# Kernel optimization log

Hardware: AMD Instinct MI355X
Metric: run time of the kernel (lower is better)

Reference implementation:

```python
import jax, jax.numpy as jnp
import numpy as np

N = 20000
E = 320000
IN = 256
H = 4
C = 64
NEG_SLOPE = 0.2


def setup_inputs() -> dict:
    key = jax.random.key(0)
    ks = jax.random.split(key, 12)
    HC = H * C

    def w(k, shape, fan_in):
        return jax.random.normal(k, shape, dtype=jnp.float32) / np.sqrt(fan_in)

    x = jax.random.normal(ks[0], (N, IN), dtype=jnp.float32)
    edge_index = jax.random.randint(ks[1], (2, E), 0, N, dtype=jnp.int64)
    return {
        "x": x,
        "edge_index": edge_index,
        "Wl1": w(ks[2], (IN, HC), IN),
        "Wr1": w(ks[3], (IN, HC), IN),
        "att1": w(ks[4], (H, C), C),
        "b1": jnp.zeros((HC,), dtype=jnp.float32),
        "Wl2": w(ks[5], (HC, HC), HC),
        "Wr2": w(ks[6], (HC, HC), HC),
        "att2": w(ks[7], (H, C), C),
        "b2": jnp.zeros((HC,), dtype=jnp.float32),
        "Wfc": w(ks[8], (HC, 2), HC),
        "bfc": jnp.zeros((2,), dtype=jnp.float32),
    }


def _gatv2(x, src, dst, Wl, Wr, att, b):
    """GATv2Conv (concat=True, share_weights=False), inference (no dropout)."""
    n = x.shape[0]
    xl = (x @ Wl).reshape(n, H, C)  # source-side projection
    xr = (x @ Wr).reshape(n, H, C)  # target-side projection
    # per-edge GATv2 score: a^T LeakyReLU(xl_j + xr_i)
    e = jax.nn.leaky_relu(xl[src] + xr[dst], NEG_SLOPE)      # [E, H, C]
    score = jnp.einsum("ehc,hc->eh", e, att)                 # [E, H]
    # segment softmax over incoming edges of each target node
    smax = jax.ops.segment_max(score, dst, num_segments=n)   # [N, H]
    ex = jnp.exp(score - smax[dst])
    denom = jax.ops.segment_sum(ex, dst, num_segments=n)     # [N, H]
    alpha = ex / denom[dst]                                  # [E, H]
    # scatter-aggregate messages (source projections weighted by alpha)
    out = jax.ops.segment_sum(alpha[:, :, None] * xl[src], dst, num_segments=n)
    return out.reshape(n, H * C) + b


def reference(x, edge_index, Wl1, Wr1, att1, b1, Wl2, Wr2, att2, b2, Wfc, bfc):
    n = x.shape[0]
    # add_self_loops=True (PyG default)
    loop = jnp.arange(n, dtype=edge_index.dtype)
    src = jnp.concatenate([edge_index[0], loop])
    dst = jnp.concatenate([edge_index[1], loop])

    h = _gatv2(x, src, dst, Wl1, Wr1, att1, b1)
    h = jax.nn.relu(h)
    h = _gatv2(h, src, dst, Wl2, Wr2, att2, b2)
    h = jax.nn.relu(h)
    g = jnp.mean(h, axis=0, keepdims=True)  # [1, H*C]
    return g @ Wfc + bfc                    # [1, 2]
```

## Files before the change

kernel.cpp:

```cpp
#include <hip/hip_runtime.h>
#include <hip/hip_bf16.h>
#include <math.h>

#define Nn 20000
#define Ee 320000
#define INF_ 256
#define Hh 4
#define Cc 64
#define HC 256
#define NB_ 79
#define NEG_SLOPE 0.2f

using frag16 = __attribute__((ext_vector_type(8))) short;
using f32x4  = __attribute__((ext_vector_type(4))) float;

__device__ __forceinline__ void async16(const void* g, void* l) {
    __builtin_amdgcn_global_load_lds(
        (const __attribute__((address_space(1))) unsigned int*)g,
        (__attribute__((address_space(3))) unsigned int*)l,
        16, 0, 0);
}


__global__ void init_deg(int* deg, float* gpart, int n) {
    int i = blockIdx.x * blockDim.x + threadIdx.x;
    if (i < n) deg[i] = 1;
    if (i < 32 * 256) gpart[i] = 0.f;
}

__global__ void hist_kernel(const int* __restrict__ dst, int ne, int* deg) {
    int e = blockIdx.x * blockDim.x + threadIdx.x;
    if (e < ne) atomicAdd(&deg[dst[e]], 1);
}

__global__ __launch_bounds__(256) void scan1(const int* __restrict__ deg,
                                             int* __restrict__ excl,
                                             int* __restrict__ bsum, int n) {
    int tid = threadIdx.x;
    int gid = blockIdx.x * 256 + tid;
    int lane = tid & 63;
    int v = (gid < n) ? deg[gid] : 0;
    int x = v;
    #pragma unroll
    for (int off = 1; off < 64; off <<= 1) {
        int y = __shfl_up(x, off, 64);
        if (lane >= off) x += y;
    }
    __shared__ int wsum[4];
    if (lane == 63) wsum[tid >> 6] = x;
    __syncthreads();
    int wadd = 0;
    for (int w = 0; w < (tid >> 6); ++w) wadd += wsum[w];
    int incl = x + wadd;
    if (gid < n) excl[gid] = incl - v;
    if (tid == 255) bsum[blockIdx.x] = incl;
}

__global__ void scan2(const int* __restrict__ bsum, int* __restrict__ boff, int nb) {
    int lane = threadIdx.x;
    int carry = 0;
    for (int base = 0; base < nb; base += 64) {
        int i = base + lane;
        int v = (i < nb) ? bsum[i] : 0;
        int x = v;
        #pragma unroll
        for (int off = 1; off < 64; off <<= 1) {
            int y = __shfl_up(x, off, 64);
            if (lane >= off) x += y;
        }
        if (i < nb) boff[i] = carry + x - v;
        carry += __shfl(x, 63, 64);
    }
    if (lane == 0) boff[nb] = carry;
}

__global__ void scan_add(int* __restrict__ row_start, int* __restrict__ cursor,
                         const int* __restrict__ boff, int n, int nb) {
    int gid = blockIdx.x * blockDim.x + threadIdx.x;
    if (gid < n) {
        int v = row_start[gid] + boff[gid >> 8];
        row_start[gid] = v;
        cursor[gid] = v;
    }
    if (gid == n) row_start[n] = boff[nb];
}

__global__ void scatter_kernel(const int* __restrict__ src, const int* __restrict__ dst,
                               int ne, int n, int* cursor, int* colx) {
    int e = blockIdx.x * blockDim.x + threadIdx.x;
    if (e < ne) {
        int d = dst[e];
        int pos = atomicAdd(&cursor[d], 1);
        colx[pos] = src[e];
    } else if (e < ne + n) {
        int node = e - ne;
        int pos = atomicAdd(&cursor[node], 1);
        colx[pos] = node;
    }
}


__device__ inline unsigned short bf16rn(float f) {
    unsigned u = __float_as_uint(f);
    unsigned r = (u + 0x7FFFu + ((u >> 16) & 1u)) >> 16;
    return (unsigned short)r;
}

__device__ inline void split1(float v, short& h, short& l) {
    unsigned short hh = bf16rn(v);
    float back = __uint_as_float(((unsigned)hh) << 16);
    unsigned short ll = bf16rn(v - back);
    h = (short)hh; l = (short)ll;
}

__device__ __forceinline__ float4 bf4_to_f4(ushort4 u) {
    return make_float4(__uint_as_float((unsigned)u.x << 16),
                       __uint_as_float((unsigned)u.y << 16),
                       __uint_as_float((unsigned)u.z << 16),
                       __uint_as_float((unsigned)u.w << 16));
}


__global__ __launch_bounds__(256) void prep(const float* __restrict__ x,
                                            const float* __restrict__ Wl1,
                                            const float* __restrict__ Wr1,
                                            const float* __restrict__ Wl2,
                                            const float* __restrict__ Wr2,
                                            short* __restrict__ Ah,
                                            short* __restrict__ Al,
                                            short* __restrict__ WhT1,
                                            short* __restrict__ WlT1,
                                            short* __restrict__ WhT2,
                                            short* __restrict__ WlT2,
                                            int n4) {
    __shared__ float T[64][65];
    int b = blockIdx.x, tid = threadIdx.x;
    if (b < 64) {
        int m  = b >> 4;
        int tr = (b >> 2) & 3;
        int tc = b & 3;
        const float* W = (m == 0) ? Wl1 : (m == 1) ? Wr1 : (m == 2) ? Wl2 : Wr2;
        short* Wh = (m < 2) ? WhT1 : WhT2;
        short* Wl = (m < 2) ? WlT1 : WlT2;
        int colofs = (m & 1) * 256;
        int lr = tid >> 4;
        int lq = (tid & 15) * 4;
        #pragma unroll
        for (int it = 0; it < 4; ++it) {
            int r = it * 16 + lr;
            float4 v = *(const float4*)&W[(size_t)(tr * 64 + r) * 256 + tc * 64 + lq];
            T[r][lq + 0] = v.x; T[r][lq + 1] = v.y;
            T[r][lq + 2] = v.z; T[r][lq + 3] = v.w;
        }
        __syncthreads();
        #pragma unroll
        for (int it = 0; it < 4; ++it) {
            int cl = it * 16 + lr;
            int kl = (tid & 15) * 4;
            short4 h, l;
            split1(T[kl + 0][cl], h.x, l.x);
            split1(T[kl + 1][cl], h.y, l.y);
            split1(T[kl + 2][cl], h.z, l.z);
            split1(T[kl + 3][cl], h.w, l.w);
            size_t o = (size_t)(colofs + tc * 64 + cl) * 256 + tr * 64 + kl;
            *(short4*)&Wh[o] = h;
            *(short4*)&Wl[o] = l;
        }
    } else {
        int i = (b - 64) * 256 + tid;
        if (i < n4) {
            float4 v = ((const float4*)x)[i];
            short4 h, l;
            split1(v.x, h.x, l.x);
            split1(v.y, h.y, l.y);
            split1(v.z, h.z, l.z);
            split1(v.w, h.w, l.w);
            ((short4*)Ah)[i] = h;
            ((short4*)Al)[i] = l;
        }
    }
}


__global__ __launch_bounds__(256, 4) void mfma_gemm(const short* __restrict__ Ah,
                                                    const short* __restrict__ Al,
                                                    const short* __restrict__ WhT,
                                                    const short* __restrict__ WlT,
                                                    unsigned short* __restrict__ XLh,
                                                    float* __restrict__ XR) {
    __shared__ short BsH[64 * 256];
    __shared__ short BsL[64 * 256];

    int tid = threadIdx.x;
    int wave = tid >> 6, lane = tid & 63;
    int quad = lane >> 4, lc = lane & 15;

    int v = blockIdx.x;
    int p = (v & 7) * 79 + (v >> 3);
    int j = p >> 3;
    int colg = p & 7;
    int cbase = (colg * 64) & 255;

    {
        int cl0 = wave * 2 + (lane >> 5);
        int kcs = (lane & 31) ^ (cl0 & 7);
        const short* srcH = WhT + (size_t)(colg * 64 + cl0) * HC + kcs * 8;
        const short* srcL = WlT + (size_t)(colg * 64 + cl0) * HC + kcs * 8;
        short* dstH = &BsH[wave * 512];
        short* dstL = &BsL[wave * 512];
        #pragma unroll
        for (int r = 0; r < 8; ++r) {
            async16(srcH + (size_t)r * 8 * HC, dstH + r * 2048);
            async16(srcL + (size_t)r * 8 * HC, dstL + r * 2048);
        }
    }
    __syncthreads();

    #pragma unroll
    for (int tt = 0; tt < 2; ++tt) {
        int rowt = j + tt * 79;
        if (rowt > 156) break;
        int bm = rowt * 128;

        int row0 = bm + wave * 32 + lc;
        int row1 = row0 + 16;
        int ca0 = (row0 < Nn) ? row0 : (Nn - 1);
        int ca1 = (row1 < Nn) ? row1 : (Nn - 1);
        const short* pa0h = Ah + (size_t)ca0 * HC + quad * 8;
        const short* pa1h = Ah + (size_t)ca1 * HC + quad * 8;
        const short* pa0l = Al + (size_t)ca0 * HC + quad * 8;
        const short* pa1l = Al + (size_t)ca1 * HC + quad * 8;

        f32x4 acc[2][4] = {};
        #pragma unroll
        for (int c = 0; c < 8; ++c) {
            int k0 = c * 32;
            frag16 a0h = *(const frag16*)(pa0h + k0);
            frag16 a1h = *(const frag16*)(pa1h + k0);
            frag16 a0l = *(const frag16*)(pa0l + k0);
            frag16 a1l = *(const frag16*)(pa1l + k0);
            int sw = ((c * 4 + quad) ^ (lc & 7)) * 8;
            frag16 bh0 = *(const frag16*)&BsH[(0 * 16 + lc) * HC + sw];
            frag16 bh1 = *(const frag16*)&BsH[(1 * 16 + lc) * HC + sw];
            frag16 bh2 = *(const frag16*)&BsH[(2 * 16 + lc) * HC + sw];
            frag16 bh3 = *(const frag16*)&BsH[(3 * 16 + lc) * HC + sw];
            frag16 bl0 = *(const frag16*)&BsL[(0 * 16 + lc) * HC + sw];
            frag16 bl1 = *(const frag16*)&BsL[(1 * 16 + lc) * HC + sw];
            frag16 bl2 = *(const frag16*)&BsL[(2 * 16 + lc) * HC + sw];
            frag16 bl3 = *(const frag16*)&BsL[(3 * 16 + lc) * HC + sw];
            acc[0][0] = __builtin_amdgcn_mfma_f32_16x16x32_bf16(bh0, a0h, acc[0][0], 0, 0, 0);
            acc[1][0] = __builtin_amdgcn_mfma_f32_16x16x32_bf16(bh0, a1h, acc[1][0], 0, 0, 0);
            acc[0][1] = __builtin_amdgcn_mfma_f32_16x16x32_bf16(bh1, a0h, acc[0][1], 0, 0, 0);
            acc[1][1] = __builtin_amdgcn_mfma_f32_16x16x32_bf16(bh1, a1h, acc[1][1], 0, 0, 0);
            acc[0][2] = __builtin_amdgcn_mfma_f32_16x16x32_bf16(bh2, a0h, acc[0][2], 0, 0, 0);
            acc[1][2] = __builtin_amdgcn_mfma_f32_16x16x32_bf16(bh2, a1h, acc[1][2], 0, 0, 0);
            acc[0][3] = __builtin_amdgcn_mfma_f32_16x16x32_bf16(bh3, a0h, acc[0][3], 0, 0, 0);
            acc[1][3] = __builtin_amdgcn_mfma_f32_16x16x32_bf16(bh3, a1h, acc[1][3], 0, 0, 0);
            acc[0][0] = __builtin_amdgcn_mfma_f32_16x16x32_bf16(bh0, a0l, acc[0][0], 0, 0, 0);
            acc[1][0] = __builtin_amdgcn_mfma_f32_16x16x32_bf16(bh0, a1l, acc[1][0], 0, 0, 0);
            acc[0][1] = __builtin_amdgcn_mfma_f32_16x16x32_bf16(bh1, a0l, acc[0][1], 0, 0, 0);
            acc[1][1] = __builtin_amdgcn_mfma_f32_16x16x32_bf16(bh1, a1l, acc[1][1], 0, 0, 0);
            acc[0][2] = __builtin_amdgcn_mfma_f32_16x16x32_bf16(bh2, a0l, acc[0][2], 0, 0, 0);
            acc[1][2] = __builtin_amdgcn_mfma_f32_16x16x32_bf16(bh2, a1l, acc[1][2], 0, 0, 0);
            acc[0][3] = __builtin_amdgcn_mfma_f32_16x16x32_bf16(bh3, a0l, acc[0][3], 0, 0, 0);
            acc[1][3] = __builtin_amdgcn_mfma_f32_16x16x32_bf16(bh3, a1l, acc[1][3], 0, 0, 0);
            acc[0][0] = __builtin_amdgcn_mfma_f32_16x16x32_bf16(bl0, a0h, acc[0][0], 0, 0, 0);
            acc[1][0] = __builtin_amdgcn_mfma_f32_16x16x32_bf16(bl0, a1h, acc[1][0], 0, 0, 0);
            acc[0][1] = __builtin_amdgcn_mfma_f32_16x16x32_bf16(bl1, a0h, acc[0][1], 0, 0, 0);
            acc[1][1] = __builtin_amdgcn_mfma_f32_16x16x32_bf16(bl1, a1h, acc[1][1], 0, 0, 0);
            acc[0][2] = __builtin_amdgcn_mfma_f32_16x16x32_bf16(bl2, a0h, acc[0][2], 0, 0, 0);
            acc[1][2] = __builtin_amdgcn_mfma_f32_16x16x32_bf16(bl2, a1h, acc[1][2], 0, 0, 0);
            acc[0][3] = __builtin_amdgcn_mfma_f32_16x16x32_bf16(bl3, a0h, acc[0][3], 0, 0, 0);
            acc[1][3] = __builtin_amdgcn_mfma_f32_16x16x32_bf16(bl3, a1h, acc[1][3], 0, 0, 0);
        }

        #pragma unroll
        for (int mt = 0; mt < 2; ++mt) {
            int rw = bm + wave * 32 + mt * 16 + lc;
            if (rw >= Nn) continue;
            #pragma unroll
            for (int t = 0; t < 4; ++t) {
                int col0 = cbase + t * 16 + quad * 4;
                if (colg < 4) {
                    ushort4 o;
                    o.x = bf16rn(acc[mt][t][0]);
                    o.y = bf16rn(acc[mt][t][1]);
                    o.z = bf16rn(acc[mt][t][2]);
                    o.w = bf16rn(acc[mt][t][3]);
                    *(ushort4*)&XLh[(size_t)rw * HC + col0] = o;
                } else {
                    *(f32x4*)&XR[(size_t)rw * HC + col0] = acc[mt][t];
                }
            }
        }
    }
}


__device__ __forceinline__ float edge_score(const float4 v, const float4 xr,
                                            const float4 a06, const float4 a04) {
    float tx = v.x + xr.x, ty = v.y + xr.y, tz = v.z + xr.z, tw = v.w + xr.w;
    float p = a06.x * tx + a04.x * fabsf(tx);
    p += a06.y * ty + a04.y * fabsf(ty);
    p += a06.z * tz + a04.z * fabsf(tz);
    p += a06.w * tw + a04.w * fabsf(tw);
    p += __shfl_xor(p, 1, 64);
    p += __shfl_xor(p, 2, 64);
    p += __shfl_xor(p, 4, 64);
    p += __shfl_xor(p, 8, 64);
    return p;
}

__global__ __launch_bounds__(256) void gat_kernel(const ushort4* __restrict__ XL4,
                                                  const float4* __restrict__ XR4,
                                                  const int* __restrict__ row_start,
                                                  const int* __restrict__ colx,
                                                  const float4* __restrict__ att4,
                                                  const float4* __restrict__ bias4,
                                                  float* __restrict__ gpart,
                                                  short4* __restrict__ Ahi,
                                                  short4* __restrict__ Alo,
                                                  int mode) {
    __shared__ float4 sred[4][64];
    int wave = threadIdx.x >> 6, lane = threadIdx.x & 63;
    int node = blockIdx.x * 4 + wave;
    float4 xr = XR4[(size_t)node * 64 + lane];
    float4 a  = att4[lane];
    float4 a06 = make_float4(a.x * 0.6f, a.y * 0.6f, a.z * 0.6f, a.w * 0.6f);
    float4 a04 = make_float4(a.x * 0.4f, a.y * 0.4f, a.z * 0.4f, a.w * 0.4f);
    int e0 = __builtin_amdgcn_readfirstlane(row_start[node]);
    int e1 = __builtin_amdgcn_readfirstlane(row_start[node + 1]);
    float l0 = 0.f, l1 = 0.f;
    float4 acc0 = make_float4(0.f, 0.f, 0.f, 0.f);
    float4 acc1 = make_float4(0.f, 0.f, 0.f, 0.f);
    int npairs = (e1 - e0) >> 1;
    int e = e0;
    int s0 = 0, s1 = 0;
    if (npairs > 0) { s0 = colx[e]; s1 = colx[e + 1]; }
    for (int pp = 0; pp < npairs; ++pp) {
        int en = e + 2;
        int i0 = (en     < e1) ? en     : (e1 - 1);
        int i1 = (en + 1 < e1) ? en + 1 : (e1 - 1);
        int ns0 = colx[i0];
        int ns1 = colx[i1];
        ushort4 u0 = XL4[(size_t)s0 * 64 + lane];
        ushort4 u1 = XL4[(size_t)s1 * 64 + lane];
        float4 v0 = bf4_to_f4(u0);
        float4 v1 = bf4_to_f4(u1);
        float pe0 = __expf(edge_score(v0, xr, a06, a04));
        float pe1 = __expf(edge_score(v1, xr, a06, a04));
        l0 += pe0; l1 += pe1;
        acc0.x += pe0 * v0.x; acc0.y += pe0 * v0.y;
        acc0.z += pe0 * v0.z; acc0.w += pe0 * v0.w;
        acc1.x += pe1 * v1.x; acc1.y += pe1 * v1.y;
        acc1.z += pe1 * v1.z; acc1.w += pe1 * v1.w;
        s0 = ns0; s1 = ns1; e = en;
    }
    if (e < e1) {
        int st = colx[e];
        float4 v0 = bf4_to_f4(XL4[(size_t)st * 64 + lane]);
        float pe0 = __expf(edge_score(v0, xr, a06, a04));
        l0 += pe0;
        acc0.x += pe0 * v0.x; acc0.y += pe0 * v0.y;
        acc0.z += pe0 * v0.z; acc0.w += pe0 * v0.w;
    }
    float rl = 1.f / (l0 + l1);
    float4 b = bias4[lane];
    float4 o = make_float4(fmaxf((acc0.x + acc1.x) * rl + b.x, 0.f),
                           fmaxf((acc0.y + acc1.y) * rl + b.y, 0.f),
                           fmaxf((acc0.z + acc1.z) * rl + b.z, 0.f),
                           fmaxf((acc0.w + acc1.w) * rl + b.w, 0.f));
    if (mode) {
        short4 h4, l4;
        split1(o.x, h4.x, l4.x);
        split1(o.y, h4.y, l4.y);
        split1(o.z, h4.z, l4.z);
        split1(o.w, h4.w, l4.w);
        size_t oidx = (size_t)node * 64 + lane;
        Ahi[oidx] = h4;
        Alo[oidx] = l4;
    } else {
        sred[wave][lane] = o;
        __syncthreads();
        if (threadIdx.x < 64) {
            int l = threadIdx.x;
            float4 s = sred[0][l];
            float4 s1v = sred[1][l], s2v = sred[2][l], s3v = sred[3][l];
            s.x += s1v.x + s2v.x + s3v.x;
            s.y += s1v.y + s2v.y + s3v.y;
            s.z += s1v.z + s2v.z + s3v.z;
            s.w += s1v.w + s2v.w + s3v.w;
            float* gp = gpart + (blockIdx.x & 31) * 256 + l * 4;
            atomicAdd(gp + 0, s.x);
            atomicAdd(gp + 1, s.y);
            atomicAdd(gp + 2, s.z);
            atomicAdd(gp + 3, s.w);
        }
    }
}


__global__ __launch_bounds__(256) void fc_kernel(const float* __restrict__ gpart,
                                                 const float* __restrict__ Wfc,
                                                 const float* __restrict__ bfc,
                                                 float* __restrict__ out, float invN) {
    int t = threadIdx.x;
    float s = 0.f;
    #pragma unroll
    for (int k = 0; k < 32; ++k) s += gpart[k * 256 + t];
    float gv = s * invN;
    float p0 = gv * Wfc[2 * t];
    float p1 = gv * Wfc[2 * t + 1];
    #pragma unroll
    for (int off = 32; off > 0; off >>= 1) {
        p0 += __shfl_xor(p0, off, 64);
        p1 += __shfl_xor(p1, off, 64);
    }
    __shared__ float s0[4], s1[4];
    if ((t & 63) == 0) { s0[t >> 6] = p0; s1[t >> 6] = p1; }
    __syncthreads();
    if (t == 0) {
        out[0] = s0[0] + s0[1] + s0[2] + s0[3] + bfc[0];
        out[1] = s1[0] + s1[1] + s1[2] + s1[3] + bfc[1];
    }
}


extern "C" void kernel_launch(void* const* d_in, const int* in_sizes, int n_in,
                              void* d_out, int out_size, void* d_ws, size_t ws_size,
                              hipStream_t stream) {
    const float* x    = (const float*)d_in[0];
    const int*   eidx = (const int*)d_in[1];
    const float* Wl1  = (const float*)d_in[2];
    const float* Wr1  = (const float*)d_in[3];
    const float* att1 = (const float*)d_in[4];
    const float* b1   = (const float*)d_in[5];
    const float* Wl2  = (const float*)d_in[6];
    const float* Wr2  = (const float*)d_in[7];
    const float* att2 = (const float*)d_in[8];
    const float* b2   = (const float*)d_in[9];
    const float* Wfc  = (const float*)d_in[10];
    const float* bfc  = (const float*)d_in[11];
    float* out = (float*)d_out;

    const int* srcv = eidx;
    const int* dstv = eidx + Ee;

    size_t NHC = (size_t)Nn * HC;
    float* XR = (float*)d_ws;
    float* gpart = XR + NHC;
    unsigned short* XLh = (unsigned short*)(gpart + 32 * 256);
    short* Ah   = (short*)(XLh + NHC);
    short* Al   = Ah + NHC;
    short* WhT1 = Al + NHC;
    short* WlT1 = WhT1 + 512 * 256;
    short* WhT2 = WlT1 + 512 * 256;
    short* WlT2 = WhT2 + 512 * 256;
    int* deg       = (int*)(WlT2 + 512 * 256);
    int* row_start = deg + Nn;
    int* cursor    = row_start + (Nn + 1);
    int* colx      = cursor + Nn;
    int* bsum      = colx + (Ee + Nn);
    int* boff      = bsum + 128;

    const int N4 = (int)(NHC / 4);

    prep<<<64 + (N4 + 255) / 256, 256, 0, stream>>>(x, Wl1, Wr1, Wl2, Wr2,
                                                    Ah, Al, WhT1, WlT1, WhT2, WlT2, N4);

    init_deg<<<(Nn + 255) / 256, 256, 0, stream>>>(deg, gpart, Nn);
    hist_kernel<<<(Ee + 255) / 256, 256, 0, stream>>>(dstv, Ee, deg);
    scan1<<<NB_, 256, 0, stream>>>(deg, row_start, bsum, Nn);
    scan2<<<1, 64, 0, stream>>>(bsum, boff, NB_);
    scan_add<<<(Nn + 256) / 256, 256, 0, stream>>>(row_start, cursor, boff, Nn, NB_);
    scatter_kernel<<<(Ee + Nn + 255) / 256, 256, 0, stream>>>(srcv, dstv, Ee, Nn, cursor, colx);

    const int GB = 8 * 79;

    mfma_gemm<<<GB, 256, 0, stream>>>(Ah, Al, WhT1, WlT1, XLh, XR);
    gat_kernel<<<Nn / 4, 256, 0, stream>>>((const ushort4*)XLh, (const float4*)XR,
                                           row_start, colx, (const float4*)att1,
                                           (const float4*)b1, gpart,
                                           (short4*)Ah, (short4*)Al, 1);

    mfma_gemm<<<GB, 256, 0, stream>>>(Ah, Al, WhT2, WlT2, XLh, XR);
    gat_kernel<<<Nn / 4, 256, 0, stream>>>((const ushort4*)XLh, (const float4*)XR,
                                           row_start, colx, (const float4*)att2,
                                           (const float4*)b2, gpart,
                                           (short4*)Ah, (short4*)Al, 0);

    fc_kernel<<<1, 256, 0, stream>>>(gpart, Wfc, bfc, out, 1.0f / Nn);
}
```

Before: 263.0 us.

## Merge scan kernels, fold init into prep, and prefetch gathered rows a pair ahead

Replaces the three-kernel degree scan with a single 1024-thread block in which each thread scans 20 elements. The degree and gpart initialisation moves into the prep kernel, removing four launches in total. The GAT aggregation loop now loads the next pair's XL rows one iteration ahead and the colx indices two ahead, to hide gather latency. The cost is a serial single-block scan and more live registers in the gather loop.

```diff
diff --git a/kernel.cpp b/kernel.cpp
--- a/kernel.cpp
+++ b/kernel.cpp
@@ -22,67 +22,49 @@
 }
 
 
-__global__ void init_deg(int* deg, float* gpart, int n) {
-    int i = blockIdx.x * blockDim.x + threadIdx.x;
-    if (i < n) deg[i] = 1;
-    if (i < 32 * 256) gpart[i] = 0.f;
-}
-
 __global__ void hist_kernel(const int* __restrict__ dst, int ne, int* deg) {
     int e = blockIdx.x * blockDim.x + threadIdx.x;
     if (e < ne) atomicAdd(&deg[dst[e]], 1);
 }
 
-__global__ __launch_bounds__(256) void scan1(const int* __restrict__ deg,
-                                             int* __restrict__ excl,
-                                             int* __restrict__ bsum, int n) {
+#define SCAN_PER 20
+__global__ __launch_bounds__(1024) void scan_all(const int* __restrict__ deg,
+                                                 int* __restrict__ row_start,
+                                                 int* __restrict__ cursor) {
     int tid = threadIdx.x;
-    int gid = blockIdx.x * 256 + tid;
-    int lane = tid & 63;
-    int v = (gid < n) ? deg[gid] : 0;
-    int x = v;
+    int lane = tid & 63, w = tid >> 6;
+    int base = tid * SCAN_PER;
+    int local[SCAN_PER];
+    int sum = 0;
+    #pragma unroll
+    for (int i = 0; i < SCAN_PER; ++i) {
+        int idx = base + i;
+        int v = (idx < Nn) ? deg[idx] : 0;
+        local[i] = sum;
+        sum += v;
+    }
+    int x = sum;
     #pragma unroll
     for (int off = 1; off < 64; off <<= 1) {
         int y = __shfl_up(x, off, 64);
         if (lane >= off) x += y;
     }
-    __shared__ int wsum[4];
-    if (lane == 63) wsum[tid >> 6] = x;
+    __shared__ int wsum[16];
+    if (lane == 63) wsum[w] = x;
     __syncthreads();
     int wadd = 0;
-    for (int w = 0; w < (tid >> 6); ++w) wadd += wsum[w];
-    int incl = x + wadd;
-    if (gid < n) excl[gid] = incl - v;
-    if (tid == 255) bsum[blockIdx.x] = incl;
-}
-
-__global__ void scan2(const int* __restrict__ bsum, int* __restrict__ boff, int nb) {
-    int lane = threadIdx.x;
-    int carry = 0;
-    for (int base = 0; base < nb; base += 64) {
-        int i = base + lane;
-        int v = (i < nb) ? bsum[i] : 0;
-        int x = v;
-        #pragma unroll
-        for (int off = 1; off < 64; off <<= 1) {
-            int y = __shfl_up(x, off, 64);
-            if (lane >= off) x += y;
-        }
-        if (i < nb) boff[i] = carry + x - v;
-        carry += __shfl(x, 63, 64);
-    }
-    if (lane == 0) boff[nb] = carry;
-}
-
-__global__ void scan_add(int* __restrict__ row_start, int* __restrict__ cursor,
-                         const int* __restrict__ boff, int n, int nb) {
-    int gid = blockIdx.x * blockDim.x + threadIdx.x;
-    if (gid < n) {
-        int v = row_start[gid] + boff[gid >> 8];
-        row_start[gid] = v;
-        cursor[gid] = v;
-    }
-    if (gid == n) row_start[n] = boff[nb];
+    for (int k = 0; k < w; ++k) wadd += wsum[k];
+    int texcl = (x - sum) + wadd;
+    #pragma unroll
+    for (int i = 0; i < SCAN_PER; ++i) {
+        int idx = base + i;
+        if (idx < Nn) {
+            int v = texcl + local[i];
+            row_start[idx] = v;
+            cursor[idx] = v;
+        }
+    }
+    if (tid == 1023) row_start[Nn] = texcl + sum;
 }
 
 __global__ void scatter_kernel(const int* __restrict__ src, const int* __restrict__ dst,
@@ -132,6 +114,8 @@
                                             short* __restrict__ WlT1,
                                             short* __restrict__ WhT2,
                                             short* __restrict__ WlT2,
+                                            int* __restrict__ deg,
+                                            float* __restrict__ gpart,
                                             int n4) {
     __shared__ float T[64][65];
     int b = blockIdx.x, tid = threadIdx.x;
@@ -168,6 +152,8 @@
         }
     } else {
         int i = (b - 64) * 256 + tid;
+        if (i < Nn) deg[i] = 1;
+        if (i < 32 * 256) gpart[i] = 0.f;
         if (i < n4) {
             float4 v = ((const float4*)x)[i];
             short4 h, l;
@@ -335,16 +321,23 @@
     float4 acc1 = make_float4(0.f, 0.f, 0.f, 0.f);
     int npairs = (e1 - e0) >> 1;
     int e = e0;
-    int s0 = 0, s1 = 0;
-    if (npairs > 0) { s0 = colx[e]; s1 = colx[e + 1]; }
+    ushort4 u0 = make_ushort4(0, 0, 0, 0), u1 = u0;
+    int na = 0, nb = 0;
+    if (npairs > 0) {
+        int sa = colx[e0], sb = colx[e0 + 1];
+        u0 = XL4[(size_t)sa * 64 + lane];
+        u1 = XL4[(size_t)sb * 64 + lane];
+        if (npairs > 1) { na = colx[e0 + 2]; nb = colx[e0 + 3]; }
+        else            { na = sa; nb = sb; }
+    }
     for (int pp = 0; pp < npairs; ++pp) {
         int en = e + 2;
-        int i0 = (en     < e1) ? en     : (e1 - 1);
-        int i1 = (en + 1 < e1) ? en + 1 : (e1 - 1);
-        int ns0 = colx[i0];
-        int ns1 = colx[i1];
-        ushort4 u0 = XL4[(size_t)s0 * 64 + lane];
-        ushort4 u1 = XL4[(size_t)s1 * 64 + lane];
+        ushort4 nu0 = XL4[(size_t)na * 64 + lane];
+        ushort4 nu1 = XL4[(size_t)nb * 64 + lane];
+        bool more2 = (pp + 2 < npairs);
+        int f0 = more2 ? en + 2 : e;
+        int f1 = more2 ? en + 3 : e;
+        int ta = colx[f0], tb = colx[f1];
         float4 v0 = bf4_to_f4(u0);
         float4 v1 = bf4_to_f4(u1);
         float pe0 = __expf(edge_score(v0, xr, a06, a04));
@@ -354,7 +347,7 @@
         acc0.z += pe0 * v0.z; acc0.w += pe0 * v0.w;
         acc1.x += pe1 * v1.x; acc1.y += pe1 * v1.y;
         acc1.z += pe1 * v1.z; acc1.w += pe1 * v1.w;
-        s0 = ns0; s1 = ns1; e = en;
+        u0 = nu0; u1 = nu1; na = ta; nb = tb; e = en;
     }
     if (e < e1) {
         int st = colx[e];
@@ -460,19 +453,15 @@
     int* row_start = deg + Nn;
     int* cursor    = row_start + (Nn + 1);
     int* colx      = cursor + Nn;
-    int* bsum      = colx + (Ee + Nn);
-    int* boff      = bsum + 128;
 
     const int N4 = (int)(NHC / 4);
 
     prep<<<64 + (N4 + 255) / 256, 256, 0, stream>>>(x, Wl1, Wr1, Wl2, Wr2,
-                                                    Ah, Al, WhT1, WlT1, WhT2, WlT2, N4);
-
-    init_deg<<<(Nn + 255) / 256, 256, 0, stream>>>(deg, gpart, Nn);
+                                                    Ah, Al, WhT1, WlT1, WhT2, WlT2,
+                                                    deg, gpart, N4);
+
     hist_kernel<<<(Ee + 255) / 256, 256, 0, stream>>>(dstv, Ee, deg);
-    scan1<<<NB_, 256, 0, stream>>>(deg, row_start, bsum, Nn);
-    scan2<<<1, 64, 0, stream>>>(bsum, boff, NB_);
-    scan_add<<<(Nn + 256) / 256, 256, 0, stream>>>(row_start, cursor, boff, Nn, NB_);
+    scan_all<<<1, 1024, 0, stream>>>(deg, row_start, cursor);
     scatter_kernel<<<(Ee + Nn + 255) / 256, 256, 0, stream>>>(srcv, dstv, Ee, Nn, cursor, colx);
 
     const int GB = 8 * 79;
```

New measurement: 271.9 us. 3.4% more time.
